# Kernel optimization log

Measured on AMD Instinct MI355X. Metric: run time of the kernel, lower is better.

Reference implementation:

```python
import jax, jax.numpy as jnp
import numpy as np

EMBED = 256
HEADS = 8
HEAD_DIM = EMBED // HEADS
FFN = 1024
EPS = 1e-5


def setup_inputs() -> dict:
    key = jax.random.key(0)
    ks = jax.random.split(key, 12)
    s = 0.02
    return {
        "x": jax.random.normal(ks[0], (2, 4096, EMBED), jnp.float32),
        "ln1_g": jnp.ones((EMBED,), jnp.float32),
        "ln1_b": jnp.zeros((EMBED,), jnp.float32),
        "ln2_g": jnp.ones((EMBED,), jnp.float32),
        "ln2_b": jnp.zeros((EMBED,), jnp.float32),
        "w_qkv": jax.random.normal(ks[1], (EMBED, 3 * EMBED), jnp.float32) * s,
        "b_qkv": jnp.zeros((3 * EMBED,), jnp.float32),
        "w_out": jax.random.normal(ks[2], (EMBED, EMBED), jnp.float32) * s,
        "b_out": jnp.zeros((EMBED,), jnp.float32),
        "w_fc1": jax.random.normal(ks[3], (EMBED, FFN), jnp.float32) * s,
        "b_fc1": jnp.zeros((FFN,), jnp.float32),
        "w_fc2": jax.random.normal(ks[4], (FFN, EMBED), jnp.float32) * s,
        "b_fc2": jnp.zeros((EMBED,), jnp.float32),
    }


def _layernorm(x, g, b):
    mu = jnp.mean(x, axis=-1, keepdims=True)
    var = jnp.mean(jnp.square(x - mu), axis=-1, keepdims=True)
    return (x - mu) * jax.lax.rsqrt(var + EPS) * g + b


def _attn(x, w_qkv, b_qkv, w_out, b_out):
    B, S, E = x.shape
    qkv = x @ w_qkv + b_qkv                      # [B,S,3E]
    q, k, v = jnp.split(qkv, 3, axis=-1)
    def heads(t):
        return t.reshape(B, S, HEADS, HEAD_DIM).transpose(0, 2, 1, 3)  # [B,H,S,D]
    q, k, v = heads(q), heads(k), heads(v)
    scores = jnp.einsum("bhsd,bhtd->bhst", q, k) / (HEAD_DIM ** 0.5)
    w = jax.nn.softmax(scores, axis=-1)
    o = jnp.einsum("bhst,bhtd->bhsd", w, v)      # [B,H,S,D]
    o = o.transpose(0, 2, 1, 3).reshape(B, S, E)
    return o @ w_out + b_out


def reference(x, ln1_g, ln1_b, ln2_g, ln2_b, w_qkv, b_qkv, w_out, b_out,
              w_fc1, b_fc1, w_fc2, b_fc2):
    # Pre-norm MHSA + residual (dropout/droppath inactive at inference)
    x = x + _attn(_layernorm(x, ln1_g, ln1_b), w_qkv, b_qkv, w_out, b_out)
    h = _layernorm(x, ln2_g, ln2_b)
    h = jax.nn.gelu(h @ w_fc1 + b_fc1, approximate=False) @ w_fc2 + b_fc2
    return x + h
```

## Files before the change

kernel.cpp:

```cpp
#include <hip/hip_runtime.h>
#include <hip/hip_bf16.h>
#include <math.h>

typedef __attribute__((ext_vector_type(8))) short bf16x8;
typedef __attribute__((ext_vector_type(4))) float f32x4;
typedef __attribute__((ext_vector_type(4))) unsigned short u16x4;

#define TOKENS 8192
#define EMB 256
#define SEQ 4096
#define NH 8
#define HD 32
#define FFN_DIM 1024

__device__ __forceinline__ unsigned short f2bf_bits(float f) {
  unsigned u = __builtin_bit_cast(unsigned, f);
  u += 0x7FFFu + ((u >> 16) & 1u);
  return (unsigned short)(u >> 16);
}

__global__ __launch_bounds__(256) void wtrans_all_kernel(
    const float* __restrict__ w_qkv, const float* __restrict__ w_out,
    const float* __restrict__ w_fc1, const float* __restrict__ w_fc2,
    unsigned short* __restrict__ t_qkv, unsigned short* __restrict__ t_out,
    unsigned short* __restrict__ t_fc1, unsigned short* __restrict__ t_fc2) {
  int id = blockIdx.x * 256 + threadIdx.x;
  const int S0 = 256 * 768, S1 = S0 + 256 * 256, S2 = S1 + 256 * 1024, S3 = S2 + 1024 * 256;
  if (id < S0) {
    int n = id / 256, kk = id - n * 256;
    t_qkv[id] = f2bf_bits(w_qkv[(size_t)kk * 768 + n]);
  } else if (id < S1) {
    int r = id - S0; int n = r / 256, kk = r - n * 256;
    t_out[r] = f2bf_bits(w_out[(size_t)kk * 256 + n]);
  } else if (id < S2) {
    int r = id - S1; int n = r / 256, kk = r - n * 256;
    t_fc1[r] = f2bf_bits(w_fc1[(size_t)kk * 1024 + n]);
  } else if (id < S3) {
    int r = id - S2; int n = r / 1024, kk = r - n * 1024;
    t_fc2[r] = f2bf_bits(w_fc2[(size_t)kk * 256 + n]);
  }
}

__global__ __launch_bounds__(256) void ln_kernel(const float* __restrict__ x,
                                                 const float* __restrict__ g,
                                                 const float* __restrict__ b,
                                                 unsigned short* __restrict__ out) {
  const int tid = threadIdx.x, lane = tid & 63, wid = tid >> 6;
  const int token = blockIdx.x * 4 + wid;
  const float4 v = *(const float4*)(x + (size_t)token * EMB + lane * 4);
  float s = v.x + v.y + v.z + v.w;
#pragma unroll
  for (int m = 1; m < 64; m <<= 1) s += __shfl_xor(s, m);
  const float mean = s * (1.f / 256.f);
  const float dx = v.x - mean, dy = v.y - mean, dz = v.z - mean, dw = v.w - mean;
  float qv = dx * dx + dy * dy + dz * dz + dw * dw;
#pragma unroll
  for (int m = 1; m < 64; m <<= 1) qv += __shfl_xor(qv, m);
  const float rinv = rsqrtf(qv * (1.f / 256.f) + 1e-5f);
  const float4 gg = *(const float4*)(g + lane * 4);
  const float4 bb = *(const float4*)(b + lane * 4);
  u16x4 ov;
  ov[0] = f2bf_bits(dx * rinv * gg.x + bb.x);
  ov[1] = f2bf_bits(dy * rinv * gg.y + bb.y);
  ov[2] = f2bf_bits(dz * rinv * gg.z + bb.z);
  ov[3] = f2bf_bits(dw * rinv * gg.w + bb.w);
  *(u16x4*)(out + (size_t)token * EMB + lane * 4) = ov;
}

template <int MODE, int BM, int BN>
__global__ __launch_bounds__(256) void gemm_kernel(
    const unsigned short* __restrict__ A, const unsigned short* __restrict__ WT,
    const float* __restrict__ bias, const float* __restrict__ resid,
    void* __restrict__ out0, void* __restrict__ out1, void* __restrict__ out2,
    int K, int N) {
  constexpr int MF = BM / 32, NF = BN / 32;
  __shared__ __align__(16) short ldsA[BM * 64];
  __shared__ __align__(16) short ldsB[BN * 64];
  const int tid = threadIdx.x;
  const int lane = tid & 63, wid = tid >> 6;
  const int llo = lane & 15, lhi = lane >> 4;
  const int m0 = blockIdx.x * BM;
  const int n0 = blockIdx.y * BN;
  const int wm = (wid >> 1) * (BM / 2), wn = (wid & 1) * (BN / 2);

  f32x4 zero4 = {0.f, 0.f, 0.f, 0.f};
  f32x4 acc[MF][NF];
#pragma unroll
  for (int i = 0; i < MF; ++i)
#pragma unroll
    for (int j = 0; j < NF; ++j) acc[i][j] = zero4;

  const int nkb = K >> 6;
  for (int kb = 0; kb < nkb; ++kb) {
#pragma unroll
    for (int p = 0; p < BM / 32; ++p) {
      int idx = p * 256 + tid;
      int r = idx >> 3, ch = idx & 7;
      bf16x8 va = *(const bf16x8*)(A + (size_t)(m0 + r) * K + kb * 64 + ch * 8);
      *(bf16x8*)&ldsA[r * 64 + ((ch ^ (r & 7)) * 8)] = va;
    }
#pragma unroll
    for (int p = 0; p < BN / 32; ++p) {
      int idx = p * 256 + tid;
      int r = idx >> 3, ch = idx & 7;
      bf16x8 vb = *(const bf16x8*)(WT + (size_t)(n0 + r) * K + kb * 64 + ch * 8);
      *(bf16x8*)&ldsB[r * 64 + ((ch ^ (r & 7)) * 8)] = vb;
    }
    __syncthreads();
#pragma unroll
    for (int ks = 0; ks < 2; ++ks) {
      bf16x8 af[MF], bfr[NF];
#pragma unroll
      for (int mf = 0; mf < MF; ++mf) {
        int r = wm + mf * 16 + llo;
        af[mf] = *(const bf16x8*)&ldsA[r * 64 + (((ks * 4 + lhi) ^ (r & 7)) * 8)];
      }
#pragma unroll
      for (int nf = 0; nf < NF; ++nf) {
        int r = wn + nf * 16 + llo;
        bfr[nf] = *(const bf16x8*)&ldsB[r * 64 + (((ks * 4 + lhi) ^ (r & 7)) * 8)];
      }
#pragma unroll
      for (int mf = 0; mf < MF; ++mf)
#pragma unroll
        for (int nf = 0; nf < NF; ++nf)
          acc[mf][nf] = __builtin_amdgcn_mfma_f32_16x16x32_bf16(af[mf], bfr[nf], acc[mf][nf], 0, 0, 0);
    }
    __syncthreads();
  }

#pragma unroll
  for (int mf = 0; mf < MF; ++mf) {
#pragma unroll
    for (int nf = 0; nf < NF; ++nf) {
      const int n = n0 + wn + nf * 16 + llo;
      const float bv = bias[n];
#pragma unroll
      for (int r = 0; r < 4; ++r) {
        const int m = m0 + wm + mf * 16 + lhi * 4 + r;
        float val = acc[mf][nf][r] + bv;
        if constexpr (MODE == 0) {
          const int part = n >> 8, rem = n & 255, h = rem >> 5, d = rem & 31;
          const int bb = m >> 12, s = m & 4095, bh = bb * 8 + h;
          unsigned short ob = f2bf_bits(val);
          if (part == 0)
            ((unsigned short*)out0)[((size_t)bh * SEQ + s) * HD + d] = ob;
          else if (part == 1)
            ((unsigned short*)out1)[((size_t)bh * SEQ + s) * HD + d] = ob;
          else
            ((unsigned short*)out2)[((size_t)bh * HD + d) * SEQ + s] = ob;
        } else if constexpr (MODE == 2) {
          float gel = 0.5f * val * (1.0f + erff(val * 0.70710678118654752f));
          ((unsigned short*)out0)[(size_t)m * N + n] = f2bf_bits(gel);
        } else {
          ((float*)out0)[(size_t)m * N + n] = val + resid[(size_t)m * N + n];
        }
      }
    }
  }
}

__global__ __launch_bounds__(256) void attn_kernel(const unsigned short* __restrict__ q,
                                                   const unsigned short* __restrict__ k,
                                                   const unsigned short* __restrict__ vT,
                                                   unsigned short* __restrict__ o) {
  __shared__ __align__(16) short plds[4][16 * 64];
  const int tid = threadIdx.x, lane = tid & 63, wid = tid >> 6;
  const int llo = lane & 15, lhi = lane >> 4;
  const int bh = blockIdx.y, qb = blockIdx.x;
  const int bb = bh >> 3, hh = bh & 7;
  const int q0 = qb * 64 + wid * 16;
  const unsigned short* qp = q + (size_t)bh * SEQ * HD;
  const unsigned short* kp = k + (size_t)bh * SEQ * HD;
  const unsigned short* vp = vT + (size_t)bh * HD * SEQ;

  f32x4 zero4 = {0.f, 0.f, 0.f, 0.f};
  bf16x8 qf = *(const bf16x8*)(qp + (size_t)(q0 + llo) * HD + lhi * 8);

  f32x4 acc[2];
  float mrun[4], lrun[4];
  acc[0] = zero4;
  acc[1] = zero4;
#pragma unroll
  for (int r = 0; r < 4; ++r) { mrun[r] = -1e30f; lrun[r] = 0.f; }

  bf16x8 kf0[4], vf0[4], kf1[4], vf1[4];

  auto load_k = [&](int tt, bf16x8(&kf)[4]) {
#pragma unroll
    for (int tf = 0; tf < 4; ++tf)
      kf[tf] = *(const bf16x8*)(kp + (size_t)(tt * 64 + tf * 16 + llo) * HD + lhi * 8);
  };
  auto load_v = [&](int tt, bf16x8(&vf)[4]) {
#pragma unroll
    for (int df = 0; df < 2; ++df)
#pragma unroll
      for (int ks = 0; ks < 2; ++ks)
        vf[df * 2 + ks] =
            *(const bf16x8*)(vp + (size_t)(df * 16 + llo) * SEQ + tt * 64 + ks * 32 + lhi * 8);
  };

  const float scale = 0.17677669529663687f;

  auto step = [&](int tt, bf16x8(&kf)[4], bf16x8(&vf)[4], bf16x8(&kn)[4], bf16x8(&vn)[4]) {
    int tn = tt + 1;
    if (tn > 63) tn = 63;
    load_k(tn, kn);
    load_v(tn, vn);
    f32x4 sc[4];
#pragma unroll
    for (int tf = 0; tf < 4; ++tf)
      sc[tf] = __builtin_amdgcn_mfma_f32_16x16x32_bf16(qf, kf[tf], zero4, 0, 0, 0);
#pragma unroll
    for (int r = 0; r < 4; ++r) {
      float rm = fmaxf(fmaxf(sc[0][r], sc[1][r]), fmaxf(sc[2][r], sc[3][r]));
      rm = fmaxf(rm, __shfl_xor(rm, 1));
      rm = fmaxf(rm, __shfl_xor(rm, 2));
      rm = fmaxf(rm, __shfl_xor(rm, 4));
      rm = fmaxf(rm, __shfl_xor(rm, 8));
      rm *= scale;
      const float mn = fmaxf(mrun[r], rm);
      const float al = __expf(mrun[r] - mn);
      mrun[r] = mn;
      float rs = 0.f;
#pragma unroll
      for (int tf = 0; tf < 4; ++tf) {
        float p = __expf(__builtin_fmaf(sc[tf][r], scale, -mn));
        sc[tf][r] = p;
        rs += p;
      }
      rs += __shfl_xor(rs, 1);
      rs += __shfl_xor(rs, 2);
      rs += __shfl_xor(rs, 4);
      rs += __shfl_xor(rs, 8);
      lrun[r] = lrun[r] * al + rs;
      acc[0][r] *= al;
      acc[1][r] *= al;
    }
#pragma unroll
    for (int tf = 0; tf < 4; ++tf)
#pragma unroll
      for (int r = 0; r < 4; ++r) {
        const int row = lhi * 4 + r;
        const int col = tf * 16 + llo;
        const int sch = (col >> 3) ^ (row & 7);
        plds[wid][row * 64 + sch * 8 + (col & 7)] =
            (short)(__builtin_bit_cast(unsigned, sc[tf][r]) >> 16);
      }
#pragma unroll
    for (int ks = 0; ks < 2; ++ks) {
      const int row = llo;
      const int sch = (ks * 4 + lhi) ^ (row & 7);
      bf16x8 pa = *(const bf16x8*)&plds[wid][row * 64 + sch * 8];
#pragma unroll
      for (int df = 0; df < 2; ++df)
        acc[df] = __builtin_amdgcn_mfma_f32_16x16x32_bf16(pa, vf[df * 2 + ks], acc[df], 0, 0, 0);
    }
  };

  load_k(0, kf0);
  load_v(0, vf0);
  for (int t2 = 0; t2 < 32; ++t2) {
    step(t2 * 2, kf0, vf0, kf1, vf1);
    step(t2 * 2 + 1, kf1, vf1, kf0, vf0);
  }

#pragma unroll
  for (int r = 0; r < 4; ++r) {
    const float rl = 1.0f / lrun[r];
    const int mrow = q0 + lhi * 4 + r;
#pragma unroll
    for (int df = 0; df < 2; ++df) {
      const float val = acc[df][r] * rl;
      o[(size_t)(bb * SEQ + mrow) * EMB + hh * 32 + df * 16 + llo] = f2bf_bits(val);
    }
  }
}

extern "C" void kernel_launch(void* const* d_in, const int* in_sizes, int n_in,
                              void* d_out, int out_size, void* d_ws, size_t ws_size,
                              hipStream_t stream) {
  const float* x = (const float*)d_in[0];
  const float* ln1_g = (const float*)d_in[1];
  const float* ln1_b = (const float*)d_in[2];
  const float* ln2_g = (const float*)d_in[3];
  const float* ln2_b = (const float*)d_in[4];
  const float* w_qkv = (const float*)d_in[5];
  const float* b_qkv = (const float*)d_in[6];
  const float* w_out = (const float*)d_in[7];
  const float* b_out = (const float*)d_in[8];
  const float* w_fc1 = (const float*)d_in[9];
  const float* b_fc1 = (const float*)d_in[10];
  const float* w_fc2 = (const float*)d_in[11];
  const float* b_fc2 = (const float*)d_in[12];
  float* out = (float*)d_out;

  char* ws = (char*)d_ws;
  size_t off = 0;
  auto alloc = [&](size_t bytes) {
    void* p = ws + off;
    off += (bytes + 255) & ~(size_t)255;
    return p;
  };
  unsigned short* wqkvT = (unsigned short*)alloc((size_t)768 * 256 * 2);
  unsigned short* woutT = (unsigned short*)alloc((size_t)256 * 256 * 2);
  unsigned short* wfc1T = (unsigned short*)alloc((size_t)1024 * 256 * 2);
  unsigned short* wfc2T = (unsigned short*)alloc((size_t)256 * 1024 * 2);
  unsigned short* ln1o = (unsigned short*)alloc((size_t)TOKENS * EMB * 2);
  unsigned short* qbuf = (unsigned short*)alloc((size_t)16 * SEQ * HD * 2);
  unsigned short* kbuf = (unsigned short*)alloc((size_t)16 * SEQ * HD * 2);
  unsigned short* vTbuf = (unsigned short*)alloc((size_t)16 * SEQ * HD * 2);
  unsigned short* obuf = (unsigned short*)alloc((size_t)TOKENS * EMB * 2);
  float* x1 = (float*)alloc((size_t)TOKENS * EMB * 4);
  unsigned short* h2 = (unsigned short*)alloc((size_t)TOKENS * EMB * 2);
  unsigned short* ffn1 = (unsigned short*)alloc((size_t)TOKENS * FFN_DIM * 2);

  dim3 blk(256);
  wtrans_all_kernel<<<dim3(3072), blk, 0, stream>>>(w_qkv, w_out, w_fc1, w_fc2,
                                                    wqkvT, woutT, wfc1T, wfc2T);

  ln_kernel<<<dim3(TOKENS / 4), blk, 0, stream>>>(x, ln1_g, ln1_b, ln1o);

  gemm_kernel<0, 128, 64><<<dim3(64, 12), blk, 0, stream>>>(ln1o, wqkvT, b_qkv, nullptr,
                                                            qbuf, kbuf, vTbuf, 256, 768);

  attn_kernel<<<dim3(64, 16), blk, 0, stream>>>(qbuf, kbuf, vTbuf, obuf);

  gemm_kernel<1, 64, 64><<<dim3(128, 4), blk, 0, stream>>>(obuf, woutT, b_out, x,
                                                           x1, nullptr, nullptr, 256, 256);

  ln_kernel<<<dim3(TOKENS / 4), blk, 0, stream>>>(x1, ln2_g, ln2_b, h2);

  gemm_kernel<2, 128, 64><<<dim3(64, 16), blk, 0, stream>>>(h2, wfc1T, b_fc1, nullptr,
                                                            ffn1, nullptr, nullptr, 256, 1024);

  gemm_kernel<3, 64, 64><<<dim3(128, 4), blk, 0, stream>>>(ffn1, wfc2T, b_fc2, x1,
                                                           out, nullptr, nullptr, 1024, 256);
}
```

Before: 319.5 us.

## Transpose QK^T in attention, prescale Q by log2e/sqrt(d), use bpermute instead of LDS

The QKV GEMM epilogue now multiplies Q by scale*log2(e) before rounding to bf16, so the attention softmax can use exp2f with no per-element scale FMA. The score MFMA is computed as K·Q^T, which gives each lane one query column. Row max and row sum then reduce over only two cross-lane shuffles, and each lane keeps a single running max and sum. The P tile is repacked into the A-operand layout with ds_bpermute instead of an LDS store/load round trip, and the V prefetch is dropped in favour of loading V at the start of each step. The extra bpermutes and the loss of V double-buffering may add latency.

```diff
diff --git a/kernel.cpp b/kernel.cpp
--- a/kernel.cpp
+++ b/kernel.cpp
@@ -5,6 +5,7 @@
 typedef __attribute__((ext_vector_type(8))) short bf16x8;
 typedef __attribute__((ext_vector_type(4))) float f32x4;
 typedef __attribute__((ext_vector_type(4))) unsigned short u16x4;
+typedef __attribute__((ext_vector_type(4))) unsigned int u32x4;
 
 #define TOKENS 8192
 #define EMB 256
@@ -13,10 +14,17 @@
 #define HD 32
 #define FFN_DIM 1024
 
+#define QK_PRESCALE 0.25503486f
+
 __device__ __forceinline__ unsigned short f2bf_bits(float f) {
   unsigned u = __builtin_bit_cast(unsigned, f);
   u += 0x7FFFu + ((u >> 16) & 1u);
   return (unsigned short)(u >> 16);
+}
+
+__device__ __forceinline__ unsigned pack_bf(float a, float b) {
+  return (__builtin_bit_cast(unsigned, a) >> 16) |
+         (__builtin_bit_cast(unsigned, b) & 0xFFFF0000u);
 }
 
 __global__ __launch_bounds__(256) void wtrans_all_kernel(
@@ -142,13 +150,14 @@
         if constexpr (MODE == 0) {
           const int part = n >> 8, rem = n & 255, h = rem >> 5, d = rem & 31;
           const int bb = m >> 12, s = m & 4095, bh = bb * 8 + h;
-          unsigned short ob = f2bf_bits(val);
-          if (part == 0)
-            ((unsigned short*)out0)[((size_t)bh * SEQ + s) * HD + d] = ob;
-          else if (part == 1)
-            ((unsigned short*)out1)[((size_t)bh * SEQ + s) * HD + d] = ob;
-          else
-            ((unsigned short*)out2)[((size_t)bh * HD + d) * SEQ + s] = ob;
+          if (part == 0) {
+            ((unsigned short*)out0)[((size_t)bh * SEQ + s) * HD + d] =
+                f2bf_bits(val * QK_PRESCALE);
+          } else if (part == 1) {
+            ((unsigned short*)out1)[((size_t)bh * SEQ + s) * HD + d] = f2bf_bits(val);
+          } else {
+            ((unsigned short*)out2)[((size_t)bh * HD + d) * SEQ + s] = f2bf_bits(val);
+          }
         } else if constexpr (MODE == 2) {
           float gel = 0.5f * val * (1.0f + erff(val * 0.70710678118654752f));
           ((unsigned short*)out0)[(size_t)m * N + n] = f2bf_bits(gel);
@@ -164,7 +173,6 @@
                                                    const unsigned short* __restrict__ k,
                                                    const unsigned short* __restrict__ vT,
                                                    unsigned short* __restrict__ o) {
-  __shared__ __align__(16) short plds[4][16 * 64];
   const int tid = threadIdx.x, lane = tid & 63, wid = tid >> 6;
   const int llo = lane & 15, lhi = lane >> 4;
   const int bh = blockIdx.y, qb = blockIdx.x;
@@ -178,20 +186,23 @@
   bf16x8 qf = *(const bf16x8*)(qp + (size_t)(q0 + llo) * HD + lhi * 8);
 
   f32x4 acc[2];
-  float mrun[4], lrun[4];
   acc[0] = zero4;
   acc[1] = zero4;
-#pragma unroll
-  for (int r = 0; r < 4; ++r) { mrun[r] = -1e30f; lrun[r] = 0.f; }
-
-  bf16x8 kf0[4], vf0[4], kf1[4], vf1[4];
+  float mrun = -3.0e38f, lrun = 0.f;
+
+  const int addr0 = 4 * (llo + 32 * (lhi & 1));
+  const int addr1 = addr0 + 64;
+  const int addrR = 4 * (lhi * 4);
+  const bool hiSel = (lhi >= 2);
+
+  bf16x8 kf0[4], kf1[4], vf[4];
 
   auto load_k = [&](int tt, bf16x8(&kf)[4]) {
 #pragma unroll
     for (int tf = 0; tf < 4; ++tf)
       kf[tf] = *(const bf16x8*)(kp + (size_t)(tt * 64 + tf * 16 + llo) * HD + lhi * 8);
   };
-  auto load_v = [&](int tt, bf16x8(&vf)[4]) {
+  auto load_v = [&](int tt) {
 #pragma unroll
     for (int df = 0; df < 2; ++df)
 #pragma unroll
@@ -200,58 +211,72 @@
             *(const bf16x8*)(vp + (size_t)(df * 16 + llo) * SEQ + tt * 64 + ks * 32 + lhi * 8);
   };
 
-  const float scale = 0.17677669529663687f;
-
-  auto step = [&](int tt, bf16x8(&kf)[4], bf16x8(&vf)[4], bf16x8(&kn)[4], bf16x8(&vn)[4]) {
+  auto step = [&](int tt, bf16x8(&kf)[4], bf16x8(&kn)[4]) {
+    load_v(tt);
+    f32x4 sc[4];
+#pragma unroll
+    for (int tf = 0; tf < 4; ++tf)
+      sc[tf] = __builtin_amdgcn_mfma_f32_16x16x32_bf16(kf[tf], qf, zero4, 0, 0, 0);
     int tn = tt + 1;
     if (tn > 63) tn = 63;
     load_k(tn, kn);
-    load_v(tn, vn);
-    f32x4 sc[4];
+
+    float m16 = fmaxf(fmaxf(sc[0][0], sc[0][1]), fmaxf(sc[0][2], sc[0][3]));
+#pragma unroll
+    for (int tf = 1; tf < 4; ++tf)
+      m16 = fmaxf(m16, fmaxf(fmaxf(sc[tf][0], sc[tf][1]), fmaxf(sc[tf][2], sc[tf][3])));
+    m16 = fmaxf(m16, __shfl_xor(m16, 16));
+    m16 = fmaxf(m16, __shfl_xor(m16, 32));
+    const float mn = fmaxf(mrun, m16);
+    const float nm = -mn;
+    const float al = exp2f(mrun - mn);
+    mrun = mn;
+
+    float rs = 0.f;
 #pragma unroll
     for (int tf = 0; tf < 4; ++tf)
-      sc[tf] = __builtin_amdgcn_mfma_f32_16x16x32_bf16(qf, kf[tf], zero4, 0, 0, 0);
-#pragma unroll
-    for (int r = 0; r < 4; ++r) {
-      float rm = fmaxf(fmaxf(sc[0][r], sc[1][r]), fmaxf(sc[2][r], sc[3][r]));
-      rm = fmaxf(rm, __shfl_xor(rm, 1));
-      rm = fmaxf(rm, __shfl_xor(rm, 2));
-      rm = fmaxf(rm, __shfl_xor(rm, 4));
-      rm = fmaxf(rm, __shfl_xor(rm, 8));
-      rm *= scale;
-      const float mn = fmaxf(mrun[r], rm);
-      const float al = __expf(mrun[r] - mn);
-      mrun[r] = mn;
-      float rs = 0.f;
-#pragma unroll
-      for (int tf = 0; tf < 4; ++tf) {
-        float p = __expf(__builtin_fmaf(sc[tf][r], scale, -mn));
+#pragma unroll
+      for (int r = 0; r < 4; ++r) {
+        float p = exp2f(sc[tf][r] + nm);
         sc[tf][r] = p;
         rs += p;
       }
-      rs += __shfl_xor(rs, 1);
-      rs += __shfl_xor(rs, 2);
-      rs += __shfl_xor(rs, 4);
-      rs += __shfl_xor(rs, 8);
-      lrun[r] = lrun[r] * al + rs;
-      acc[0][r] *= al;
-      acc[1][r] *= al;
-    }
-#pragma unroll
-    for (int tf = 0; tf < 4; ++tf)
-#pragma unroll
-      for (int r = 0; r < 4; ++r) {
-        const int row = lhi * 4 + r;
-        const int col = tf * 16 + llo;
-        const int sch = (col >> 3) ^ (row & 7);
-        plds[wid][row * 64 + sch * 8 + (col & 7)] =
-            (short)(__builtin_bit_cast(unsigned, sc[tf][r]) >> 16);
-      }
+    rs += __shfl_xor(rs, 16);
+    rs += __shfl_xor(rs, 32);
+    lrun = lrun * al + rs;
+
+#pragma unroll
+    for (int r = 0; r < 4; ++r) {
+      float alr = __builtin_bit_cast(
+          float, __builtin_amdgcn_ds_bpermute(addrR + 4 * r,
+                                              __builtin_bit_cast(int, al)));
+      acc[0][r] *= alr;
+      acc[1][r] *= alr;
+    }
+
+    unsigned w[4][2];
+#pragma unroll
+    for (int tf = 0; tf < 4; ++tf) {
+      w[tf][0] = pack_bf(sc[tf][0], sc[tf][1]);
+      w[tf][1] = pack_bf(sc[tf][2], sc[tf][3]);
+    }
+
 #pragma unroll
     for (int ks = 0; ks < 2; ++ks) {
-      const int row = llo;
-      const int sch = (ks * 4 + lhi) ^ (row & 7);
-      bf16x8 pa = *(const bf16x8*)&plds[wid][row * 64 + sch * 8];
+      int aL0 = __builtin_amdgcn_ds_bpermute(addr0, (int)w[2 * ks][0]);
+      int bL0 = __builtin_amdgcn_ds_bpermute(addr0, (int)w[2 * ks + 1][0]);
+      int aL1 = __builtin_amdgcn_ds_bpermute(addr0, (int)w[2 * ks][1]);
+      int bL1 = __builtin_amdgcn_ds_bpermute(addr0, (int)w[2 * ks + 1][1]);
+      int aH0 = __builtin_amdgcn_ds_bpermute(addr1, (int)w[2 * ks][0]);
+      int bH0 = __builtin_amdgcn_ds_bpermute(addr1, (int)w[2 * ks + 1][0]);
+      int aH1 = __builtin_amdgcn_ds_bpermute(addr1, (int)w[2 * ks][1]);
+      int bH1 = __builtin_amdgcn_ds_bpermute(addr1, (int)w[2 * ks + 1][1]);
+      u32x4 c;
+      c[0] = (unsigned)(hiSel ? bL0 : aL0);
+      c[1] = (unsigned)(hiSel ? bL1 : aL1);
+      c[2] = (unsigned)(hiSel ? bH0 : aH0);
+      c[3] = (unsigned)(hiSel ? bH1 : aH1);
+      bf16x8 pa = __builtin_bit_cast(bf16x8, c);
 #pragma unroll
       for (int df = 0; df < 2; ++df)
         acc[df] = __builtin_amdgcn_mfma_f32_16x16x32_bf16(pa, vf[df * 2 + ks], acc[df], 0, 0, 0);
@@ -259,19 +284,21 @@
   };
 
   load_k(0, kf0);
-  load_v(0, vf0);
   for (int t2 = 0; t2 < 32; ++t2) {
-    step(t2 * 2, kf0, vf0, kf1, vf1);
-    step(t2 * 2 + 1, kf1, vf1, kf0, vf0);
-  }
-
+    step(t2 * 2, kf0, kf1);
+    step(t2 * 2 + 1, kf1, kf0);
+  }
+
+  const float rl = 1.0f / lrun;
 #pragma unroll
   for (int r = 0; r < 4; ++r) {
-    const float rl = 1.0f / lrun[r];
+    float rlr = __builtin_bit_cast(
+        float, __builtin_amdgcn_ds_bpermute(addrR + 4 * r,
+                                            __builtin_bit_cast(int, rl)));
     const int mrow = q0 + lhi * 4 + r;
 #pragma unroll
     for (int df = 0; df < 2; ++df) {
-      const float val = acc[df][r] * rl;
+      const float val = acc[df][r] * rlr;
       o[(size_t)(bb * SEQ + mrow) * EMB + hh * 32 + df * 16 + llo] = f2bf_bits(val);
     }
   }
```

Result: faster. 312.9 us (-2.1%).
